# Optimization experiments

Hardware: AMD Instinct MI355X
Metric: run time of the kernel (lower is better)

The kernel has to match this reference:

```python
import jax, jax.numpy as jnp
import numpy as np

# Last adaptive-conv stage of AdaBIGGAN (BigGAN-128): ch=96 at 128x128, hypernet input dim 148
B, C, H, W, IN = 32, 96, 128, 128, 148


def setup_inputs() -> dict:
    key = jax.random.key(0)
    k0, k1, k2, k3, k4, k5 = jax.random.split(key, 6)
    s = 0.02  # small init scale for hypernetwork linears
    return {
        "h": jax.random.normal(k0, (B, C, H, W), jnp.float32),      # feature map after cond-BN
        "y": jax.random.normal(k1, (B, IN), jnp.float32),           # [shared_embed | z-chunk] cond vector
        "Wg_w": jax.random.normal(k2, (C * C, IN), jnp.float32) * s,  # nn.Linear(148, C*C).weight
        "Wg_b": jax.random.normal(k3, (C * C,), jnp.float32) * s,     # nn.Linear(148, C*C).bias
        "Bg_w": jax.random.normal(k4, (C, IN), jnp.float32) * s,      # nn.Linear(148, C).weight
        "Bg_b": jax.random.normal(k5, (C,), jnp.float32) * s,         # nn.Linear(148, C).bias
    }


def reference(h, y, Wg_w, Wg_b, Bg_w, Bg_b):
    Bn, Cn = h.shape[0], h.shape[1]
    # hypernetwork: per-sample 1x1-conv weight [B, C, C] and bias [B, C]
    w = (y @ Wg_w.T + Wg_b).reshape(Bn, Cn, Cn)
    b = y @ Bg_w.T + Bg_b
    # Faithful to the torch broadcasting: (h[:, :, None] * w[:, :, :, None, None]).sum(2)
    # which collapses exactly to h * w.sum(-1), avoiding the [B,C,C,H,W] blowup.
    scale = w.sum(-1)  # [B, C]
    out = h * scale[:, :, None, None] + b[:, :, None, None]
    return jax.nn.relu(out)  # block.activation1
```

## Files before the change

kernel.cpp:

```cpp
#include <hip/hip_runtime.h>
#include <stdint.h>

#define B_  32
#define C_  96
#define HW_ 16384
#define IN_ 148

typedef float f32x4 __attribute__((ext_vector_type(4)));

__global__ __launch_bounds__(512) void hyper_kernel(
    const float* __restrict__ Wg_w, const float* __restrict__ Wg_b,
    const float* __restrict__ Bg_w, const float* __restrict__ Bg_b,
    const float* __restrict__ y,
    float* __restrict__ scale, float* __restrict__ bias) {
    const int c   = blockIdx.x;
    const int tid = threadIdx.x;

    __shared__ float sW2[2][IN_];
    __shared__ float sW[IN_];
    __shared__ float sB[IN_];
    __shared__ float sWbS;

    if (tid < 2 * IN_) {
        const int half = (tid >= IN_) ? 1 : 0;
        const int col  = tid - half * IN_;
        const float* p = Wg_w + (size_t)c * C_ * IN_ + (size_t)(half * 48) * IN_ + col;
        float s = 0.f;
        #pragma unroll 4
        for (int j = 0; j < 48; ++j) s += p[(size_t)j * IN_];
        sW2[half][col] = s;
        if (half == 0) sB[col] = Bg_w[c * IN_ + col];
    }
    if (tid < 64) {
        float v = Wg_b[c * C_ + tid];
        if (tid < C_ - 64) v += Wg_b[c * C_ + 64 + tid];
        #pragma unroll
        for (int off = 32; off > 0; off >>= 1) v += __shfl_down(v, off);
        if (tid == 0) sWbS = v;
    }
    __syncthreads();
    if (tid < IN_) sW[tid] = sW2[0][tid] + sW2[1][tid];
    __syncthreads();

    const int wave = tid >> 6, lane = tid & 63;
    for (int b = wave; b < B_; b += 8) {
        float y0 = y[b * IN_ + lane];
        float y1 = y[b * IN_ + 64 + lane];
        float ps = y0 * sW[lane] + y1 * sW[64 + lane];
        float pb = y0 * sB[lane] + y1 * sB[64 + lane];
        if (lane < IN_ - 128) {
            float y2 = y[b * IN_ + 128 + lane];
            ps += y2 * sW[128 + lane];
            pb += y2 * sB[128 + lane];
        }
        #pragma unroll
        for (int off = 32; off > 0; off >>= 1) {
            ps += __shfl_down(ps, off);
            pb += __shfl_down(pb, off);
        }
        if (lane == 0) {
            scale[b * C_ + c] = ps + sWbS;
            bias [b * C_ + c] = pb + Bg_b[c];
        }
    }
}

__global__ __launch_bounds__(256) void apply_kernel(
    const float* __restrict__ h, const float* __restrict__ scale,
    const float* __restrict__ bias, float* __restrict__ out) {
    const int cidx  = blockIdx.x * 256 + threadIdx.x;
    const int plane = cidx >> 11;

    const float s  = scale[plane];
    const float bb = bias[plane];

    const f32x4* hp = reinterpret_cast<const f32x4*>(h) + (size_t)cidx * 2;
    f32x4*       op = reinterpret_cast<f32x4*>(out)     + (size_t)cidx * 2;

    f32x4 v0 = __builtin_nontemporal_load(hp);
    f32x4 v1 = __builtin_nontemporal_load(hp + 1);
    f32x4 o0, o1;
    #pragma unroll
    for (int k = 0; k < 4; ++k) {
        o0[k] = fmaxf(fmaf(v0[k], s, bb), 0.f);
        o1[k] = fmaxf(fmaf(v1[k], s, bb), 0.f);
    }
    __builtin_nontemporal_store(o0, op);
    __builtin_nontemporal_store(o1, op + 1);
}

extern "C" void kernel_launch(void* const* d_in, const int* in_sizes, int n_in,
                              void* d_out, int out_size, void* d_ws, size_t ws_size,
                              hipStream_t stream) {
    const float* h    = (const float*)d_in[0];
    const float* y    = (const float*)d_in[1];
    const float* Wg_w = (const float*)d_in[2];
    const float* Wg_b = (const float*)d_in[3];
    const float* Bg_w = (const float*)d_in[4];
    const float* Bg_b = (const float*)d_in[5];
    float* out = (float*)d_out;

    float* scale = (float*)d_ws;
    float* bias  = scale + B_ * C_;

    hyper_kernel<<<C_, 512, 0, stream>>>(Wg_w, Wg_b, Bg_w, Bg_b, y, scale, bias);

    const int nchunk = (B_ * C_ * HW_) / 8;
    apply_kernel<<<nchunk / 256, 256, 0, stream>>>(h, scale, bias, out);
}
```

Measured before the change: 348.9 us.

## Fuse hypernetwork reduction into the per-plane scale/bias/ReLU apply kernel

Replaces the two-kernel pipeline (hypernet kernel writing scale/bias to workspace, then elementwise apply) with a single kernel where each block owns one (b,c) plane. Each block recomputes its plane's scale and bias by dotting the 96x148 slice of Wg_w with y, then streams the 16384-element plane. This removes a kernel launch and the serial dependency between the tiny hypernet kernel and the bandwidth-bound apply. The cost is redundant weight reads: each channel's Wg_w slice is reread by 32 blocks, mostly from L2, plus a modulo index per element and extra block syncs before streaming starts.

```diff
diff --git a/kernel.cpp b/kernel.cpp
--- a/kernel.cpp
+++ b/kernel.cpp
@@ -5,88 +5,71 @@
 #define C_  96
 #define HW_ 16384
 #define IN_ 148
+#define WROWS_ (C_ * IN_)
 
 typedef float f32x4 __attribute__((ext_vector_type(4)));
 
-__global__ __launch_bounds__(512) void hyper_kernel(
+__global__ __launch_bounds__(256) void fused_kernel(
+    const float* __restrict__ h, const float* __restrict__ y,
     const float* __restrict__ Wg_w, const float* __restrict__ Wg_b,
     const float* __restrict__ Bg_w, const float* __restrict__ Bg_b,
-    const float* __restrict__ y,
-    float* __restrict__ scale, float* __restrict__ bias) {
-    const int c   = blockIdx.x;
-    const int tid = threadIdx.x;
+    float* __restrict__ out) {
+    const int plane = blockIdx.x;
+    const int b     = plane / C_;
+    const int c     = plane - b * C_;
+    const int tid   = threadIdx.x;
 
-    __shared__ float sW2[2][IN_];
-    __shared__ float sW[IN_];
-    __shared__ float sB[IN_];
-    __shared__ float sWbS;
+    __shared__ float ys[IN_];
+    __shared__ float red_s[4], red_b[4];
+    __shared__ float sSB[2];
 
-    if (tid < 2 * IN_) {
-        const int half = (tid >= IN_) ? 1 : 0;
-        const int col  = tid - half * IN_;
-        const float* p = Wg_w + (size_t)c * C_ * IN_ + (size_t)(half * 48) * IN_ + col;
-        float s = 0.f;
+    if (tid < IN_) ys[tid] = y[b * IN_ + tid];
+    __syncthreads();
+
+    float ps = 0.f, pb = 0.f;
+    {
+        const float* wp = Wg_w + (size_t)c * WROWS_;
         #pragma unroll 4
-        for (int j = 0; j < 48; ++j) s += p[(size_t)j * IN_];
-        sW2[half][col] = s;
-        if (half == 0) sB[col] = Bg_w[c * IN_ + col];
+        for (int e = tid; e < WROWS_; e += 256) {
+            ps += wp[e] * ys[e % IN_];
+        }
+        if (tid < C_)  ps += Wg_b[c * C_ + tid];
+        if (tid < IN_) pb  = ys[tid] * Bg_w[c * IN_ + tid];
+        if (tid == 0)  pb += Bg_b[c];
     }
-    if (tid < 64) {
-        float v = Wg_b[c * C_ + tid];
-        if (tid < C_ - 64) v += Wg_b[c * C_ + 64 + tid];
-        #pragma unroll
-        for (int off = 32; off > 0; off >>= 1) v += __shfl_down(v, off);
-        if (tid == 0) sWbS = v;
+    #pragma unroll
+    for (int off = 32; off > 0; off >>= 1) {
+        ps += __shfl_down(ps, off);
+        pb += __shfl_down(pb, off);
+    }
+    const int wave = tid >> 6, lane = tid & 63;
+    if (lane == 0) { red_s[wave] = ps; red_b[wave] = pb; }
+    __syncthreads();
+    if (tid == 0) {
+        sSB[0] = red_s[0] + red_s[1] + red_s[2] + red_s[3];
+        sSB[1] = red_b[0] + red_b[1] + red_b[2] + red_b[3];
     }
     __syncthreads();
-    if (tid < IN_) sW[tid] = sW2[0][tid] + sW2[1][tid];
-    __syncthreads();
+    const float s  = sSB[0];
+    const float bb = sSB[1];
 
-    const int wave = tid >> 6, lane = tid & 63;
-    for (int b = wave; b < B_; b += 8) {
-        float y0 = y[b * IN_ + lane];
-        float y1 = y[b * IN_ + 64 + lane];
-        float ps = y0 * sW[lane] + y1 * sW[64 + lane];
-        float pb = y0 * sB[lane] + y1 * sB[64 + lane];
-        if (lane < IN_ - 128) {
-            float y2 = y[b * IN_ + 128 + lane];
-            ps += y2 * sW[128 + lane];
-            pb += y2 * sB[128 + lane];
+    const size_t c4base = (size_t)plane * (HW_ / 4);
+    const f32x4* hp4 = reinterpret_cast<const f32x4*>(h);
+    f32x4*       op4 = reinterpret_cast<f32x4*>(out);
+    #pragma unroll
+    for (int it = 0; it < 8; ++it) {
+        const size_t i4 = c4base + (size_t)(it * 256 + tid) * 2;
+        f32x4 v0 = __builtin_nontemporal_load(hp4 + i4);
+        f32x4 v1 = __builtin_nontemporal_load(hp4 + i4 + 1);
+        f32x4 o0, o1;
+        #pragma unroll
+        for (int k = 0; k < 4; ++k) {
+            o0[k] = fmaxf(fmaf(v0[k], s, bb), 0.f);
+            o1[k] = fmaxf(fmaf(v1[k], s, bb), 0.f);
         }
-        #pragma unroll
-        for (int off = 32; off > 0; off >>= 1) {
-            ps += __shfl_down(ps, off);
-            pb += __shfl_down(pb, off);
-        }
-        if (lane == 0) {
-            scale[b * C_ + c] = ps + sWbS;
-            bias [b * C_ + c] = pb + Bg_b[c];
-        }
+        __builtin_nontemporal_store(o0, op4 + i4);
+        __builtin_nontemporal_store(o1, op4 + i4 + 1);
     }
-}
-
-__global__ __launch_bounds__(256) void apply_kernel(
-    const float* __restrict__ h, const float* __restrict__ scale,
-    const float* __restrict__ bias, float* __restrict__ out) {
-    const int cidx  = blockIdx.x * 256 + threadIdx.x;
-    const int plane = cidx >> 11;
-
-    const float s  = scale[plane];
-    const float bb = bias[plane];
-
-    const f32x4* hp = reinterpret_cast<const f32x4*>(h) + (size_t)cidx * 2;
-    f32x4*       op = reinterpret_cast<f32x4*>(out)     + (size_t)cidx * 2;
-
-    f32x4 v0 = __builtin_nontemporal_load(hp);
-    f32x4 v1 = __builtin_nontemporal_load(hp + 1);
-    f32x4 o0, o1;
-    #pragma unroll
-    for (int k = 0; k < 4; ++k) {
-        o0[k] = fmaxf(fmaf(v0[k], s, bb), 0.f);
-        o1[k] = fmaxf(fmaf(v1[k], s, bb), 0.f);
-    }
-    __builtin_nontemporal_store(o0, op);
-    __builtin_nontemporal_store(o1, op + 1);
 }
 
 extern "C" void kernel_launch(void* const* d_in, const int* in_sizes, int n_in,
@@ -100,11 +83,5 @@
     const float* Bg_b = (const float*)d_in[5];
     float* out = (float*)d_out;
 
-    float* scale = (float*)d_ws;
-    float* bias  = scale + B_ * C_;
-
-    hyper_kernel<<<C_, 512, 0, stream>>>(Wg_w, Wg_b, Bg_w, Bg_b, y, scale, bias);
-
-    const int nchunk = (B_ * C_ * HW_) / 8;
-    apply_kernel<<<nchunk / 256, 256, 0, stream>>>(h, scale, bias, out);
+    fused_kernel<<<B_ * C_, 256, 0, stream>>>(h, y, Wg_w, Wg_b, Bg_w, Bg_b, out);
 }
```

Result: slower. 356.1 us (+2.1%).
